# Performance work log

Measured on AMD Instinct MI355X. Metric: run time of the kernel, lower is better.

Reference implementation:

```python
import jax, jax.numpy as jnp
import numpy as np

L, H, NH, I = 6, 768, 12, 3072
DH = H // NH
EPS = 1e-12


def setup_inputs() -> dict:
    key = jax.random.key(0)
    ks = jax.random.split(key, 17)
    B, S = 16, 512
    s = lambda k, shape, fan: jax.random.normal(k, shape, jnp.float32) * (1.0 / np.sqrt(fan))
    return {
        "hidden_states": jax.random.normal(ks[0], (B, S, H), jnp.float32),
        "Wq": s(ks[1], (L, H, H), H), "bq": jnp.zeros((L, H), jnp.float32),
        "Wk": s(ks[2], (L, H, H), H), "bk": jnp.zeros((L, H), jnp.float32),
        "Wv": s(ks[3], (L, H, H), H), "bv": jnp.zeros((L, H), jnp.float32),
        "Wo": s(ks[4], (L, H, H), H), "bo": jnp.zeros((L, H), jnp.float32),
        "g1": jnp.ones((L, H), jnp.float32), "b1": jnp.zeros((L, H), jnp.float32),
        "Wi": s(ks[5], (L, H, I), H), "bi": jnp.zeros((L, I), jnp.float32),
        "Wo2": s(ks[6], (L, I, H), I), "bo2": jnp.zeros((L, H), jnp.float32),
        "g2": jnp.ones((L, H), jnp.float32), "b2": jnp.zeros((L, H), jnp.float32),
    }


def _layernorm(x, g, b):
    m = jnp.mean(x, axis=-1, keepdims=True)
    v = jnp.mean(jnp.square(x - m), axis=-1, keepdims=True)
    return (x - m) * jax.lax.rsqrt(v + EPS) * g + b


def _encoder(h, params):
    def layer_fn(h, p):
        Wq, bq, Wk, bk, Wv, bv, Wo, bo, g1, b1, Wi, bi, Wo2, bo2, g2, b2 = p
        B, S, _ = h.shape
        q = (h @ Wq + bq).reshape(B, S, NH, DH)
        k = (h @ Wk + bk).reshape(B, S, NH, DH)
        v = (h @ Wv + bv).reshape(B, S, NH, DH)
        scores = jnp.einsum("bshd,bthd->bhst", q, k) / np.sqrt(DH).astype(np.float32)
        probs = jax.nn.softmax(scores, axis=-1)  # dropout is identity in eval
        ctx = jnp.einsum("bhst,bthd->bshd", probs, v).reshape(B, S, H)
        attn_out = _layernorm(ctx @ Wo + bo + h, g1, b1)
        inter = jax.nn.gelu(attn_out @ Wi + bi, approximate=False)
        out = _layernorm(inter @ Wo2 + bo2 + attn_out, g2, b2)
        return out, None

    h, _ = jax.lax.scan(layer_fn, h, params)
    return h


def reference(hidden_states, Wq, bq, Wk, bk, Wv, bv, Wo, bo, g1, b1, Wi, bi, Wo2, bo2, g2, b2):
    params = (Wq, bq, Wk, bk, Wv, bv, Wo, bo, g1, b1, Wi, bi, Wo2, bo2, g2, b2)
    return _encoder(hidden_states, params)
```

## Files before the change

kernel.cpp:

```cpp
#include <hip/hip_runtime.h>
#include <hip/hip_bf16.h>
#include <math.h>

#define LNUM  6
#define HDIM  768
#define NHEAD 12
#define DHEAD 64
#define IDIM  3072
#define NB    16
#define SEQ   512
#define MTOK  (NB*SEQ)
#define NQKV  (3*HDIM)

typedef __bf16 bf16;
typedef __bf16 bf16x4 __attribute__((ext_vector_type(4)));
typedef __bf16 bf16x8 __attribute__((ext_vector_type(8)));
typedef float  f32x4  __attribute__((ext_vector_type(4)));

__device__ __forceinline__ void async_copy16(const bf16* g, bf16* l) {
  __builtin_amdgcn_global_load_lds((__attribute__((address_space(1))) void*)g,
                                   (__attribute__((address_space(3))) void*)l,
                                   16, 0, 0);
}

__device__ __forceinline__ float gelu_fast(float t) {
  const float u = 0.7978845608f * (t + 0.044715f * t * t * t);
  const float e = __expf(-2.f * fabsf(u));
  const float th = (1.f - e) / (1.f + e);
  return 0.5f * t * (1.f + copysignf(th, u));
}

__global__ void detect_k(const unsigned short* __restrict__ probe, int* __restrict__ flag)
{
  __shared__ int sc[4];
  const int tid = threadIdx.x;
  int cnt = 0;
#pragma unroll
  for (int j = 0; j < 16; j++) {
    const unsigned short w = probe[tid * 16 + j];
    const int e = (w >> 7) & 0xFF;
    cnt += (e >= 90 && e <= 130) ? 1 : 0;
  }
#pragma unroll
  for (int o = 32; o; o >>= 1) cnt += __shfl_xor(cnt, o);
  if ((tid & 63) == 0) sc[tid >> 6] = cnt;
  __syncthreads();
  if (tid == 0) flag[0] = ((sc[0] + sc[1] + sc[2] + sc[3]) < 3482) ? 1 : 0;
}

__global__ void cvt1d_k(const void* __restrict__ src, bf16* __restrict__ dst,
                        int n, const int* __restrict__ flag)
{
  const int i = blockIdx.x * 256 + threadIdx.x;
  if (i < n)
    dst[i] = (*flag) ? (bf16)((const float*)src)[i] : ((const bf16*)src)[i];
}

__global__ void cvt_slice_k(const void* __restrict__ src, bf16* __restrict__ dst,
                            int perL, int off, int dstStride, int total,
                            const int* __restrict__ flag)
{
  const int i = blockIdx.x * 256 + threadIdx.x;
  if (i < total) {
    const int l = i / perL, c = i - l * perL;
    const bf16 v = (*flag) ? (bf16)((const float*)src)[i] : ((const bf16*)src)[i];
    dst[l * dstStride + off + c] = v;
  }
}

__global__ void wtrans_k(const void* __restrict__ src, bf16* __restrict__ dst,
                         int K, int N, int layer, int dstLS, int dstOff,
                         const int* __restrict__ flag)
{
  __shared__ bf16 t[32][33];
  const size_t sOff = (size_t)(blockIdx.z + layer) * K * N;
  const size_t dOff = (size_t)blockIdx.z * dstLS + dstOff;
  const int n0 = blockIdx.x * 32, k0 = blockIdx.y * 32;
  const int tx = threadIdx.x, ty = threadIdx.y;
  const int f = *flag;
#pragma unroll
  for (int i = 0; i < 4; i++) {
    const size_t idx = sOff + (size_t)(k0 + ty*4 + i) * N + n0 + tx;
    t[ty*4+i][tx] = f ? (bf16)((const float*)src)[idx] : ((const bf16*)src)[idx];
  }
  __syncthreads();
#pragma unroll
  for (int i = 0; i < 4; i++)
    dst[dOff + (size_t)(n0 + ty*4 + i) * K + k0 + tx] = t[tx][ty*4+i];
}

template<int BM, int BN, int MT, int NT, int EPI, int XS>
__global__ __launch_bounds__(256)
void gemm_bt(const bf16* __restrict__ A, const bf16* __restrict__ Bt,
             float* __restrict__ Cf, bf16* __restrict__ Cb,
             bf16* __restrict__ Cb2, bf16* __restrict__ Cb3,
             const bf16* __restrict__ bias, const bf16* __restrict__ res,
             int K, int sA, int sB, int sC)
{
  __shared__ __align__(16) bf16 ldsA[BM*32];
  __shared__ __align__(16) bf16 ldsB[BN*32];
  const int tid  = threadIdx.x;
  const int wave = tid >> 6;
  const int lane = tid & 63;
  const int quad = lane >> 4;
  const int l16  = lane & 15;
  const int wm = wave >> 1, wn = wave & 1;
  const int swz = (l16 >> 1) & 3;

  int bx = blockIdx.x, by = blockIdx.y;
  if (XS) {
    if ((gridDim.y & 7) == 0) {
      const int id  = by * gridDim.x + bx;
      const int xcd = id & 7, slot = id >> 3;
      bx = slot % gridDim.x;
      by = (slot / gridDim.x) * 8 + xcd;
    }
  }
  const int m0 = by * BM;
  const int n0 = bx * BN;
  const int srow = tid >> 2;
  const int scol = (((tid & 3) ^ ((tid >> 3) & 3))) * 8;

  const bf16* gA = A + (size_t)(m0 + srow) * sA + scol;
  const bf16* gB = Bt + (size_t)(n0 + srow) * sB + scol;
  bf16* lA = &ldsA[(wave * 16) * 32];
  bf16* lB = &ldsB[(wave * 16) * 32];

  f32x4 acc[MT][NT];
  const f32x4 fzero = {0.f, 0.f, 0.f, 0.f};
#pragma unroll
  for (int i = 0; i < MT; i++)
#pragma unroll
    for (int j = 0; j < NT; j++) acc[i][j] = fzero;

  for (int k0 = 0; k0 < K; k0 += 32) {
#pragma unroll
    for (int p = 0; p < BM/64; p++)
      async_copy16(gA + (size_t)p * 64 * sA + k0, lA + p * 64 * 32);
#pragma unroll
    for (int p = 0; p < BN/64; p++)
      async_copy16(gB + (size_t)p * 64 * sB + k0, lB + p * 64 * 32);
    __syncthreads();

    bf16x8 af[MT], bfv[NT];
#pragma unroll
    for (int i = 0; i < MT; i++)
      af[i] = *(const bf16x8*)&ldsA[(wm*(MT*16) + i*16 + l16) * 32 + (quad ^ swz) * 8];
#pragma unroll
    for (int j = 0; j < NT; j++)
      bfv[j] = *(const bf16x8*)&ldsB[(wn*(NT*16) + j*16 + l16) * 32 + (quad ^ swz) * 8];
#pragma unroll
    for (int i = 0; i < MT; i++)
#pragma unroll
      for (int j = 0; j < NT; j++)
        acc[i][j] = __builtin_amdgcn_mfma_f32_16x16x32_bf16(af[i], bfv[j], acc[i][j], 0, 0, 0);
    __syncthreads();
  }

#pragma unroll
  for (int i = 0; i < MT; i++) {
    const int mtile = m0 + wm*(MT*16) + i*16 + quad*4;
#pragma unroll
    for (int j = 0; j < NT; j++) {
      const int nn = n0 + wn*(NT*16) + j*16 + l16;
      const float bv = bias ? (float)bias[nn] : 0.f;
      if (EPI == 5) {
        if (nn < HDIM) {
#pragma unroll
          for (int r = 0; r < 4; r++)
            Cb[(size_t)(mtile + r) * HDIM + nn] = (bf16)((acc[i][j][r] + bv) * 0.125f);
        } else if (nn < 2*HDIM) {
#pragma unroll
          for (int r = 0; r < 4; r++)
            Cb2[(size_t)(mtile + r) * HDIM + (nn - HDIM)] = (bf16)(acc[i][j][r] + bv);
        } else {
          const int nn2 = nn - 2*HDIM;
          const int bb = mtile >> 9, s = mtile & 511;
          const int hh = nn2 >> 6, dd = nn2 & 63;
          const size_t base = ((size_t)(bb*NHEAD + hh) * DHEAD + dd) * SEQ + s;
          bf16x4 pk;
#pragma unroll
          for (int r = 0; r < 4; r++) pk[r] = (bf16)(acc[i][j][r] + bv);
          *(bf16x4*)(Cb3 + base) = pk;
        }
      } else {
#pragma unroll
        for (int r = 0; r < 4; r++) {
          const int mm = mtile + r;
          const size_t idx = (size_t)mm * sC + nn;
          const float v = acc[i][j][r];
          if (EPI == 2) Cf[idx] = v + bv + (float)res[idx];
          else if (EPI == 3) Cb[idx] = (bf16)gelu_fast(v + bv);
        }
      }
    }
  }
}

#define STG_A(DST, h, kt2) do {                                               \
    async_copy16(gA + (size_t)((h)*128     ) * sA + (size_t)(kt2)*64,         \
                 &DST[(h)*8192 +        tid*8]);                              \
    async_copy16(gA + (size_t)((h)*128 + 64) * sA + (size_t)(kt2)*64,         \
                 &DST[(h)*8192 + 4096 + tid*8]);                              \
  } while (0)

#define STG_B(DST, h, kt2) do {                                               \
    async_copy16(gB + (size_t)((h)*128     ) * sB + (size_t)(kt2)*64,         \
                 &DST[(h)*8192 +        tid*8]);                              \
    async_copy16(gB + (size_t)((h)*128 + 64) * sB + (size_t)(kt2)*64,         \
                 &DST[(h)*8192 + 4096 + tid*8]);                              \
  } while (0)

#define MFMA16(ACI0, BREG, NOFF)                                              \
  __builtin_amdgcn_s_setprio(1);                                              \
  _Pragma("unroll")                                                           \
  for (int ks = 0; ks < 2; ks++)                                              \
    _Pragma("unroll")                                                         \
    for (int f = 0; f < 4; f++)                                               \
      _Pragma("unroll")                                                       \
      for (int nf = 0; nf < 2; nf++)                                          \
        acc[(ACI0) + f][(NOFF) + nf] =                                        \
            __builtin_amdgcn_mfma_f32_16x16x32_bf16(                          \
                aF[ks][f], BREG[ks][nf], acc[(ACI0) + f][(NOFF) + nf], 0,0,0);\
  __builtin_amdgcn_s_setprio(0);

#define DO_KTILE(AC, BC, STG0, STG1, STG2, STG3, ENDW)                        \
  {                                                                           \
                \
    _Pragma("unroll")                                                         \
    for (int f = 0; f < 4; f++) {                                             \
      const int row = (wm*128 + f*16 + l16) * 64;                             \
      aF[0][f] = *(const bf16x8*)&AC[row + sl0*8];                            \
      aF[1][f] = *(const bf16x8*)&AC[row + sl1*8];                            \
    }                                                                         \
    _Pragma("unroll")                                                         \
    for (int nf = 0; nf < 2; nf++) {                                          \
      const int row = (wn*64 + nf*16 + l16) * 64;                             \
      bA[0][nf] = *(const bf16x8*)&BC[row + sl0*8];                           \
      bA[1][nf] = *(const bf16x8*)&BC[row + sl1*8];                           \
    }                                                                         \
    STG0;                                                                     \
    asm volatile("s_waitcnt lgkmcnt(8)" ::: "memory");                        \
    __builtin_amdgcn_s_barrier();                                             \
    asm volatile("s_waitcnt lgkmcnt(0)" ::: "memory");                        \
    MFMA16(0, bA, 0)                                                          \
    __builtin_amdgcn_s_barrier();                                             \
                                    \
    _Pragma("unroll")                                                         \
    for (int nf = 0; nf < 2; nf++) {                                          \
      const int row = (wn*64 + 32 + nf*16 + l16) * 64;                        \
      bB[0][nf] = *(const bf16x8*)&BC[row + sl0*8];                           \
      bB[1][nf] = *(const bf16x8*)&BC[row + sl1*8];                           \
    }                                                                         \
    STG1;                                                                     \
    __builtin_amdgcn_s_barrier();                                             \
    asm volatile("s_waitcnt lgkmcnt(0)" ::: "memory");                        \
    MFMA16(0, bB, 2)                                                          \
    __builtin_amdgcn_s_barrier();                                             \
                          \
    _Pragma("unroll")                                                         \
    for (int f = 0; f < 4; f++) {                                             \
      const int row = (wm*128 + 64 + f*16 + l16) * 64;                        \
      aF[0][f] = *(const bf16x8*)&AC[row + sl0*8];                            \
      aF[1][f] = *(const bf16x8*)&AC[row + sl1*8];                            \
    }                                                                         \
    STG2;                                                                     \
    __builtin_amdgcn_s_barrier();                                             \
    asm volatile("s_waitcnt lgkmcnt(0)" ::: "memory");                        \
    MFMA16(4, bB, 2)                                                          \
    __builtin_amdgcn_s_barrier();                                             \
                                            \
    STG3;                                                                     \
    __builtin_amdgcn_s_barrier();                                             \
    MFMA16(4, bA, 0)                                                          \
    ENDW;                                                                     \
    __builtin_amdgcn_s_barrier();                                             \
  }

template<int EPI>
__global__ __launch_bounds__(512, 2)
void gemm256(const bf16* __restrict__ A, const bf16* __restrict__ Bt,
             float* __restrict__ Cf, bf16* __restrict__ Cb,
             bf16* __restrict__ Cb2, bf16* __restrict__ Cb3,
             const bf16* __restrict__ bias, const bf16* __restrict__ res,
             int K, int sA, int sB, int sC)
{
  __shared__ __align__(16) bf16 As0[256*64];
  __shared__ __align__(16) bf16 As1[256*64];
  __shared__ __align__(16) bf16 Bs0[256*64];
  __shared__ __align__(16) bf16 Bs1[256*64];

  const int tid  = threadIdx.x;
  const int wave = tid >> 6;
  const int lane = tid & 63;
  const int quad = lane >> 4;
  const int l16  = lane & 15;
  const int wm   = wave >> 2;
  const int wn   = wave & 3;

  int bx = blockIdx.x, by = blockIdx.y;
  if ((gridDim.y & 7) == 0) {
    const int id  = by * gridDim.x + bx;
    const int xcd = id & 7, slot = id >> 3;
    bx = slot % gridDim.x;
    by = (slot / gridDim.x) * 8 + xcd;
  }
  const int m0 = by * 256;
  const int n0 = bx * 256;

  const int rb  = tid >> 3;
  const int sb  = tid & 7;
  const int sbx = sb ^ (rb & 7);
  const bf16* gA = A  + (size_t)(m0 + rb) * sA + sbx * 8;
  const bf16* gB = Bt + (size_t)(n0 + rb) * sB + sbx * 8;

  const int s7  = l16 & 7;
  const int sl0 = (0 + quad) ^ s7;
  const int sl1 = (4 + quad) ^ s7;

  f32x4 acc[8][4];
  const f32x4 fzero = {0.f, 0.f, 0.f, 0.f};
#pragma unroll
  for (int i = 0; i < 8; i++)
#pragma unroll
    for (int j = 0; j < 4; j++) acc[i][j] = fzero;

  bf16x8 aF[2][4], bA[2][2], bB[2][2];

  const int NKT = K >> 6;

  STG_A(As0, 0, 0); STG_A(As0, 1, 0);
  STG_B(Bs0, 0, 0); STG_B(Bs0, 1, 0);
  if (NKT > 1) { STG_B(Bs1, 0, 1); STG_B(Bs1, 1, 1); }
  if (NKT > 1) asm volatile("s_waitcnt vmcnt(4)" ::: "memory");
  else         asm volatile("s_waitcnt vmcnt(0)" ::: "memory");
  __builtin_amdgcn_s_barrier();

  for (int kt = 0; kt < NKT; kt += 2) {
    const bool s2 = (kt + 2 < NKT);
    const bool s3 = (kt + 3 < NKT);
    DO_KTILE(As0, Bs0,
             STG_A(As1, 0, kt + 1),
             STG_A(As1, 1, kt + 1),
             if (s2) STG_B(Bs0, 0, kt + 2),
             if (s2) STG_B(Bs0, 1, kt + 2),
             if (s2) { asm volatile("s_waitcnt vmcnt(4)" ::: "memory"); }
             else    { asm volatile("s_waitcnt vmcnt(0)" ::: "memory"); })
    DO_KTILE(As1, Bs1,
             if (s2) STG_A(As0, 0, kt + 2),
             if (s2) STG_A(As0, 1, kt + 2),
             if (s3) STG_B(Bs1, 0, kt + 3),
             if (s3) STG_B(Bs1, 1, kt + 3),
             if (s2) { asm volatile("s_waitcnt vmcnt(4)" ::: "memory"); })
  }

#pragma unroll
  for (int mf = 0; mf < 8; mf++) {
    const int mtile = m0 + wm*128 + mf*16 + quad*4;
#pragma unroll
    for (int nf = 0; nf < 4; nf++) {
      const int nn = n0 + wn*64 + nf*16 + l16;
      const float bv = bias ? (float)bias[nn] : 0.f;
      if (EPI == 5) {
        if (nn < HDIM) {
#pragma unroll
          for (int r = 0; r < 4; r++)
            Cb[(size_t)(mtile + r) * HDIM + nn] = (bf16)((acc[mf][nf][r] + bv) * 0.125f);
        } else if (nn < 2*HDIM) {
#pragma unroll
          for (int r = 0; r < 4; r++)
            Cb2[(size_t)(mtile + r) * HDIM + (nn - HDIM)] = (bf16)(acc[mf][nf][r] + bv);
        } else {
          const int nn2 = nn - 2*HDIM;
          const int bb = mtile >> 9, s = mtile & 511;
          const int hh = nn2 >> 6, dd = nn2 & 63;
          const size_t base = ((size_t)(bb*NHEAD + hh) * DHEAD + dd) * SEQ + s;
          bf16x4 pk;
#pragma unroll
          for (int r = 0; r < 4; r++) pk[r] = (bf16)(acc[mf][nf][r] + bv);
          *(bf16x4*)(Cb3 + base) = pk;
        }
      } else if (EPI == 3) {
#pragma unroll
        for (int r = 0; r < 4; r++)
          Cb[(size_t)(mtile + r) * sC + nn] = (bf16)gelu_fast(acc[mf][nf][r] + bv);
      } else if (EPI == 2) {
#pragma unroll
        for (int r = 0; r < 4; r++) {
          const size_t idx = (size_t)(mtile + r) * sC + nn;
          Cf[idx] = acc[mf][nf][r] + bv + (float)res[idx];
        }
      }
    }
  }
}

__global__ __launch_bounds__(256)
void flash_k(const bf16* __restrict__ qb, const bf16* __restrict__ kb,
             const bf16* __restrict__ vt, bf16* __restrict__ ctxb)
{
  __shared__ __align__(16) bf16 Qs[128][72];
  __shared__ __align__(16) bf16 Ks[64][72];
  __shared__ __align__(16) bf16 Vs[64][72];
  __shared__ __align__(16) bf16 Ps[128][72];
  const int tid = threadIdx.x;
  const int wave = tid >> 6, lane = tid & 63;
  const int quad = lane >> 4, l16 = lane & 15;
  const int z = blockIdx.y;
  const int b = z / NHEAD, h = z - b * NHEAD;
  const int qt = blockIdx.x;
  const size_t qRow0 = (size_t)b * SEQ + qt * 128;

#pragma unroll
  for (int r = 0; r < 4; r++) {
    const int idx = tid + r * 256;
    const int row = idx >> 3, c8 = (idx & 7) * 8;
    *(bf16x8*)&Qs[row][c8] =
        *(const bf16x8*)&qb[(qRow0 + row) * HDIM + h * DHEAD + c8];
  }

  f32x4 Oacc[2][4];
  float mrow[2][4], lrow[2][4];
#pragma unroll
  for (int i = 0; i < 2; i++)
#pragma unroll
    for (int n = 0; n < 4; n++) Oacc[i][n] = (f32x4){0.f,0.f,0.f,0.f};
#pragma unroll
  for (int i = 0; i < 2; i++)
#pragma unroll
    for (int r = 0; r < 4; r++) { mrow[i][r] = -3.0e38f; lrow[i][r] = 0.f; }

  for (int j = 0; j < 8; j++) {
    __syncthreads();
#pragma unroll
    for (int r = 0; r < 2; r++) {
      const int idx = tid + r * 256;
      const int row = idx >> 3, c8 = (idx & 7) * 8;
      *(bf16x8*)&Ks[row][c8] =
          *(const bf16x8*)&kb[((size_t)b*SEQ + j*64 + row) * HDIM + h*DHEAD + c8];
      *(bf16x8*)&Vs[row][c8] =
          *(const bf16x8*)&vt[((size_t)z*DHEAD + row) * SEQ + j*64 + c8];
    }
    __syncthreads();

    f32x4 Sacc[2][4];
#pragma unroll
    for (int i = 0; i < 2; i++)
#pragma unroll
      for (int n = 0; n < 4; n++) Sacc[i][n] = (f32x4){0.f,0.f,0.f,0.f};
#pragma unroll
    for (int kk = 0; kk < 2; kk++) {
      bf16x8 af[2], bv[4];
#pragma unroll
      for (int i = 0; i < 2; i++)
        af[i] = *(const bf16x8*)&Qs[wave*32 + i*16 + l16][kk*32 + quad*8];
#pragma unroll
      for (int n = 0; n < 4; n++)
        bv[n] = *(const bf16x8*)&Ks[n*16 + l16][kk*32 + quad*8];
#pragma unroll
      for (int i = 0; i < 2; i++)
#pragma unroll
        for (int n = 0; n < 4; n++)
          Sacc[i][n] = __builtin_amdgcn_mfma_f32_16x16x32_bf16(af[i], bv[n], Sacc[i][n], 0,0,0);
    }

    float alpha[2][4];
#pragma unroll
    for (int i = 0; i < 2; i++)
#pragma unroll
      for (int r = 0; r < 4; r++) {
        float mx = Sacc[i][0][r];
#pragma unroll
        for (int n = 1; n < 4; n++) mx = fmaxf(mx, Sacc[i][n][r]);
#pragma unroll
        for (int o = 8; o; o >>= 1) mx = fmaxf(mx, __shfl_xor(mx, o));
        const float mn = fmaxf(mrow[i][r], mx);
        const float a = __expf(mrow[i][r] - mn);
        float rs = 0.f;
#pragma unroll
        for (int n = 0; n < 4; n++) {
          const float p = __expf(Sacc[i][n][r] - mn);
          Sacc[i][n][r] = p; rs += p;
        }
#pragma unroll
        for (int o = 8; o; o >>= 1) rs += __shfl_xor(rs, o);
        lrow[i][r] = lrow[i][r] * a + rs;
        mrow[i][r] = mn;
        alpha[i][r] = a;
      }

#pragma unroll
    for (int i = 0; i < 2; i++)
#pragma unroll
      for (int n = 0; n < 4; n++)
#pragma unroll
        for (int r = 0; r < 4; r++)
          Ps[wave*32 + i*16 + quad*4 + r][n*16 + l16] = (bf16)Sacc[i][n][r];
    __syncthreads();

#pragma unroll
    for (int i = 0; i < 2; i++)
#pragma unroll
      for (int n = 0; n < 4; n++)
#pragma unroll
        for (int r = 0; r < 4; r++) Oacc[i][n][r] *= alpha[i][r];
#pragma unroll
    for (int kk = 0; kk < 2; kk++) {
      bf16x8 af[2], bv[4];
#pragma unroll
      for (int i = 0; i < 2; i++)
        af[i] = *(const bf16x8*)&Ps[wave*32 + i*16 + l16][kk*32 + quad*8];
#pragma unroll
      for (int n = 0; n < 4; n++)
        bv[n] = *(const bf16x8*)&Vs[n*16 + l16][kk*32 + quad*8];
#pragma unroll
      for (int i = 0; i < 2; i++)
#pragma unroll
        for (int n = 0; n < 4; n++)
          Oacc[i][n] = __builtin_amdgcn_mfma_f32_16x16x32_bf16(af[i], bv[n], Oacc[i][n], 0,0,0);
    }
  }

#pragma unroll
  for (int i = 0; i < 2; i++)
#pragma unroll
    for (int r = 0; r < 4; r++) {
      const float inv = 1.f / lrow[i][r];
      const size_t tok = qRow0 + wave*32 + i*16 + quad*4 + r;
#pragma unroll
      for (int n = 0; n < 4; n++)
        ctxb[tok * HDIM + h*DHEAD + n*16 + l16] = (bf16)(Oacc[i][n][r] * inv);
    }
}

__global__ void layernorm_k(const float* __restrict__ x, const bf16* __restrict__ g,
                            const bf16* __restrict__ b, bf16* __restrict__ yb,
                            void* __restrict__ dout, int last, const int* __restrict__ flag)
{
  __shared__ float sred[4];
  const int row = blockIdx.x;
  const int tid = threadIdx.x;
  const float* xr = x + (size_t)row * HDIM;
  const float v0 = xr[tid], v1 = xr[tid+256], v2 = xr[tid+512];
  float s = v0 + v1 + v2;
#pragma unroll
  for (int o = 32; o; o >>= 1) s += __shfl_xor(s, o);
  if ((tid & 63) == 0) sred[tid >> 6] = s;
  __syncthreads();
  const float mean = (sred[0]+sred[1]+sred[2]+sred[3]) * (1.f/768.f);
  __syncthreads();
  const float d0 = v0-mean, d1 = v1-mean, d2 = v2-mean;
  float vs = d0*d0 + d1*d1 + d2*d2;
#pragma unroll
  for (int o = 32; o; o >>= 1) vs += __shfl_xor(vs, o);
  if ((tid & 63) == 0) sred[tid >> 6] = vs;
  __syncthreads();
  const float var = (sred[0]+sred[1]+sred[2]+sred[3]) * (1.f/768.f);
  const float rs  = rsqrtf(var + 1e-12f);
  const float y0 = d0*rs*(float)g[tid]     + (float)b[tid];
  const float y1 = d1*rs*(float)g[tid+256] + (float)b[tid+256];
  const float y2 = d2*rs*(float)g[tid+512] + (float)b[tid+512];
  bf16* ybr = yb + (size_t)row * HDIM;
  ybr[tid]     = (bf16)y0;
  ybr[tid+256] = (bf16)y1;
  ybr[tid+512] = (bf16)y2;
  if (last) {
    if (*flag) {
      float* o = (float*)dout + (size_t)row * HDIM;
      o[tid] = y0; o[tid+256] = y1; o[tid+512] = y2;
    } else {
      bf16* o = (bf16*)dout + (size_t)row * HDIM;
      o[tid] = (bf16)y0; o[tid+256] = (bf16)y1; o[tid+512] = (bf16)y2;
    }
  }
}

extern "C" void kernel_launch(void* const* d_in, const int* in_sizes, int n_in,
                              void* d_out, int out_size, void* d_ws, size_t ws_size,
                              hipStream_t stream)
{
  (void)in_sizes; (void)n_in; (void)out_size;

  char* ws = (char*)d_ws;
  size_t off = 0;
  auto carve = [&](size_t bytes) -> char* {
    char* p = ws + off; off += (bytes + 255) & ~(size_t)255; return p;
  };
  int*   flag = (int*)carve(256);
  bf16*  hcur = (bf16*)carve((size_t)MTOK*HDIM*2);
  bf16*  qb   = (bf16*)carve((size_t)MTOK*HDIM*2);
  bf16*  kb   = (bf16*)carve((size_t)MTOK*HDIM*2);
  bf16*  vt   = (bf16*)carve((size_t)MTOK*HDIM*2);
  bf16*  ctxb = (bf16*)carve((size_t)MTOK*HDIM*2);
  float* x1   = (float*)carve((size_t)MTOK*HDIM*4);
  bf16*  aob  = kb;

  bf16* nbqkv = (bf16*)carve((size_t)LNUM*NQKV*2);
  bf16* nbo   = (bf16*)carve((size_t)LNUM*HDIM*2);
  bf16* ng1   = (bf16*)carve((size_t)LNUM*HDIM*2);
  bf16* nb1   = (bf16*)carve((size_t)LNUM*HDIM*2);
  bf16* nbi   = (bf16*)carve((size_t)LNUM*IDIM*2);
  bf16* nbo2  = (bf16*)carve((size_t)LNUM*HDIM*2);
  bf16* ng2   = (bf16*)carve((size_t)LNUM*HDIM*2);
  bf16* nb2   = (bf16*)carve((size_t)LNUM*HDIM*2);

  const size_t wAllBytes = (size_t)LNUM*(NQKV*HDIM + HDIM*HDIM + 2*HDIM*IDIM)*2;
  const bool preAll = ws_size >= off + wAllBytes + (size_t)256*IDIM*2 + (1u<<20);
  bf16 *wqkvt=0, *wot=0, *wit=0, *wo2t=0, *bufA=0, *bufB=0;
  if (preAll) {
    wqkvt = (bf16*)carve((size_t)LNUM*NQKV*HDIM*2);
    wot   = (bf16*)carve((size_t)LNUM*HDIM*HDIM*2);
    wit   = (bf16*)carve((size_t)LNUM*HDIM*IDIM*2);
    wo2t  = (bf16*)carve((size_t)LNUM*HDIM*IDIM*2);
  } else {
    bufA = (bf16*)carve((size_t)HDIM*IDIM*2);
    bufB = (bf16*)carve((size_t)HDIM*IDIM*2);
  }

  const size_t unionAvail = (ws_size > off) ? (ws_size - off) : 0;
  int RM = 256;
  { const int rms[6] = {8192,4096,2048,1024,512,256};
    for (int i = 0; i < 6; i++)
      if ((size_t)rms[i]*IDIM*2 <= unionAvail) { RM = rms[i]; break; } }
  bf16* interb = (bf16*)(ws + off);

  detect_k<<<1, 256, 0, stream>>>((const unsigned short*)d_in[1], flag);
  cvt1d_k<<<(MTOK*HDIM+255)/256, 256, 0, stream>>>(d_in[0], hcur, MTOK*HDIM, flag);
  cvt_slice_k<<<(LNUM*HDIM+255)/256, 256, 0, stream>>>(d_in[2], nbqkv, HDIM, 0,      NQKV, LNUM*HDIM, flag);
  cvt_slice_k<<<(LNUM*HDIM+255)/256, 256, 0, stream>>>(d_in[4], nbqkv, HDIM, HDIM,   NQKV, LNUM*HDIM, flag);
  cvt_slice_k<<<(LNUM*HDIM+255)/256, 256, 0, stream>>>(d_in[6], nbqkv, HDIM, 2*HDIM, NQKV, LNUM*HDIM, flag);
  cvt1d_k<<<(LNUM*HDIM+255)/256, 256, 0, stream>>>(d_in[8],  nbo,  LNUM*HDIM, flag);
  cvt1d_k<<<(LNUM*HDIM+255)/256, 256, 0, stream>>>(d_in[9],  ng1,  LNUM*HDIM, flag);
  cvt1d_k<<<(LNUM*HDIM+255)/256, 256, 0, stream>>>(d_in[10], nb1,  LNUM*HDIM, flag);
  cvt1d_k<<<(LNUM*IDIM+255)/256, 256, 0, stream>>>(d_in[12], nbi,  LNUM*IDIM, flag);
  cvt1d_k<<<(LNUM*HDIM+255)/256, 256, 0, stream>>>(d_in[14], nbo2, LNUM*HDIM, flag);
  cvt1d_k<<<(LNUM*HDIM+255)/256, 256, 0, stream>>>(d_in[15], ng2,  LNUM*HDIM, flag);
  cvt1d_k<<<(LNUM*HDIM+255)/256, 256, 0, stream>>>(d_in[16], nb2,  LNUM*HDIM, flag);

  const dim3 tb(32, 8);
  if (preAll) {
    wtrans_k<<<dim3(HDIM/32, HDIM/32, LNUM), tb, 0, stream>>>(d_in[1], wqkvt, HDIM, HDIM, 0, NQKV*HDIM, 0,           flag);
    wtrans_k<<<dim3(HDIM/32, HDIM/32, LNUM), tb, 0, stream>>>(d_in[3], wqkvt, HDIM, HDIM, 0, NQKV*HDIM, HDIM*HDIM,   flag);
    wtrans_k<<<dim3(HDIM/32, HDIM/32, LNUM), tb, 0, stream>>>(d_in[5], wqkvt, HDIM, HDIM, 0, NQKV*HDIM, 2*HDIM*HDIM, flag);
    wtrans_k<<<dim3(HDIM/32, HDIM/32, LNUM), tb, 0, stream>>>(d_in[7], wot,  HDIM, HDIM, 0, HDIM*HDIM, 0, flag);
    wtrans_k<<<dim3(IDIM/32, HDIM/32, LNUM), tb, 0, stream>>>(d_in[11], wit,  HDIM, IDIM, 0, HDIM*IDIM, 0, flag);
    wtrans_k<<<dim3(HDIM/32, IDIM/32, LNUM), tb, 0, stream>>>(d_in[13], wo2t, IDIM, HDIM, 0, HDIM*IDIM, 0, flag);
  }

  for (int l = 0; l < LNUM; l++) {
    const bf16* hin = hcur;

    const bf16* WqkvT;
    if (preAll) WqkvT = wqkvt + (size_t)l * NQKV * HDIM;
    else {
      wtrans_k<<<dim3(HDIM/32, HDIM/32, 1), tb, 0, stream>>>(d_in[1], bufA, HDIM, HDIM, l, 0, 0,           flag);
      wtrans_k<<<dim3(HDIM/32, HDIM/32, 1), tb, 0, stream>>>(d_in[3], bufA, HDIM, HDIM, l, 0, HDIM*HDIM,   flag);
      wtrans_k<<<dim3(HDIM/32, HDIM/32, 1), tb, 0, stream>>>(d_in[5], bufA, HDIM, HDIM, l, 0, 2*HDIM*HDIM, flag);
      WqkvT = bufA;
    }
    gemm256<5><<<dim3(NQKV/256, MTOK/256), 512, 0, stream>>>(
        hin, WqkvT, nullptr, qb, kb, vt, nbqkv + (size_t)l*NQKV, nullptr,
        HDIM, HDIM, HDIM, HDIM);

    flash_k<<<dim3(SEQ/128, NB*NHEAD), 256, 0, stream>>>(qb, kb, vt, ctxb);

    const bf16* WoT;
    if (preAll) WoT = wot + (size_t)l * HDIM * HDIM;
    else {
      wtrans_k<<<dim3(HDIM/32, HDIM/32, 1), tb, 0, stream>>>(d_in[7], bufA, HDIM, HDIM, l, 0, 0, flag);
      WoT = bufA;
    }
    gemm_bt<128,128,4,4,2,1><<<dim3(HDIM/128, MTOK/128), 256, 0, stream>>>(
        ctxb, WoT, x1, nullptr, nullptr, nullptr, nbo + l*HDIM, hin,
        HDIM, HDIM, HDIM, HDIM);
    layernorm_k<<<MTOK, 256, 0, stream>>>(x1, ng1 + l*HDIM, nb1 + l*HDIM, aob,
                                          d_out, 0, flag);

    const bf16 *WiT, *Wo2T;
    if (preAll) { WiT = wit + (size_t)l*HDIM*IDIM; Wo2T = wo2t + (size_t)l*HDIM*IDIM; }
    else {
      wtrans_k<<<dim3(IDIM/32, HDIM/32, 1), tb, 0, stream>>>(d_in[11], bufA, HDIM, IDIM, l, 0, 0, flag);
      wtrans_k<<<dim3(HDIM/32, IDIM/32, 1), tb, 0, stream>>>(d_in[13], bufB, IDIM, HDIM, l, 0, 0, flag);
      WiT = bufA; Wo2T = bufB;
    }
    for (int r0 = 0; r0 < MTOK; r0 += RM) {
      gemm256<3><<<dim3(IDIM/256, RM/256), 512, 0, stream>>>(
          aob + (size_t)r0*HDIM, WiT, nullptr, interb, nullptr, nullptr,
          nbi + (size_t)l*IDIM, nullptr, HDIM, HDIM, HDIM, IDIM);
      gemm_bt<128,128,4,4,2,1><<<dim3(HDIM/128, RM/128), 256, 0, stream>>>(
          interb, Wo2T, x1 + (size_t)r0*HDIM, nullptr, nullptr, nullptr,
          nbo2 + l*HDIM, aob + (size_t)r0*HDIM, IDIM, IDIM, IDIM, HDIM);
    }
    layernorm_k<<<MTOK, 256, 0, stream>>>(x1, ng2 + l*HDIM, nb2 + l*HDIM, hcur,
                                          d_out, (l == LNUM-1) ? 1 : 0, flag);
  }
}
```

Baseline: 2.215 ms.

## Double-buffer gemm_bt LDS and replace gemm256 with it for QKV and FFN-up

Adds a two-stage LDS ping-pong to gemm_bt, so async global-to-LDS copies for the next K slice are issued before the MFMAs on the current slice, hiding load latency. It then deletes the hand-scheduled 256x256 gemm256 kernel and routes the QKV and FFN-up GEMMs through the 128x128 gemm_bt instead. This trades the larger tile's data reuse and fine-grained barrier schedule for a simpler kernel with more blocks. The loop assumes K is a multiple of 64.

```diff
diff --git a/kernel.cpp b/kernel.cpp
--- a/kernel.cpp
+++ b/kernel.cpp
@@ -89,6 +89,35 @@
     dst[dOff + (size_t)(n0 + ty*4 + i) * K + k0 + tx] = t[tx][ty*4+i];
 }
 
+#define STAGE2(DA, DB, KK) do {                                                \
+    _Pragma("unroll")                                                          \
+    for (int p = 0; p < BM/64; p++)                                            \
+      async_copy16(gA + (size_t)p * 64 * sA + (KK),                            \
+                   &DA[(wave*16)*32 + p*64*32]);                               \
+    _Pragma("unroll")                                                          \
+    for (int p = 0; p < BN/64; p++)                                            \
+      async_copy16(gB + (size_t)p * 64 * sB + (KK),                            \
+                   &DB[(wave*16)*32 + p*64*32]);                               \
+  } while (0)
+
+#define COMP2(SA, SB) do {                                                     \
+    bf16x8 af[MT], bfv[NT];                                                    \
+    _Pragma("unroll")                                                          \
+    for (int i = 0; i < MT; i++)                                               \
+      af[i] = *(const bf16x8*)&SA[(wm*(MT*16) + i*16 + l16) * 32               \
+                                  + (quad ^ swz) * 8];                         \
+    _Pragma("unroll")                                                          \
+    for (int j = 0; j < NT; j++)                                               \
+      bfv[j] = *(const bf16x8*)&SB[(wn*(NT*16) + j*16 + l16) * 32              \
+                                   + (quad ^ swz) * 8];                        \
+    _Pragma("unroll")                                                          \
+    for (int i = 0; i < MT; i++)                                               \
+      _Pragma("unroll")                                                        \
+      for (int j = 0; j < NT; j++)                                             \
+        acc[i][j] = __builtin_amdgcn_mfma_f32_16x16x32_bf16(                   \
+            af[i], bfv[j], acc[i][j], 0, 0, 0);                                \
+  } while (0)
+
 template<int BM, int BN, int MT, int NT, int EPI, int XS>
 __global__ __launch_bounds__(256)
 void gemm_bt(const bf16* __restrict__ A, const bf16* __restrict__ Bt,
@@ -97,8 +126,10 @@
              const bf16* __restrict__ bias, const bf16* __restrict__ res,
              int K, int sA, int sB, int sC)
 {
-  __shared__ __align__(16) bf16 ldsA[BM*32];
-  __shared__ __align__(16) bf16 ldsB[BN*32];
+  __shared__ __align__(16) bf16 A0[BM*32];
+  __shared__ __align__(16) bf16 B0[BN*32];
+  __shared__ __align__(16) bf16 A1[BM*32];
+  __shared__ __align__(16) bf16 B1[BN*32];
   const int tid  = threadIdx.x;
   const int wave = tid >> 6;
   const int lane = tid & 63;
@@ -123,8 +154,6 @@
 
   const bf16* gA = A + (size_t)(m0 + srow) * sA + scol;
   const bf16* gB = Bt + (size_t)(n0 + srow) * sB + scol;
-  bf16* lA = &ldsA[(wave * 16) * 32];
-  bf16* lB = &ldsB[(wave * 16) * 32];
 
   f32x4 acc[MT][NT];
   const f32x4 fzero = {0.f, 0.f, 0.f, 0.f};
@@ -133,27 +162,14 @@
 #pragma unroll
     for (int j = 0; j < NT; j++) acc[i][j] = fzero;
 
-  for (int k0 = 0; k0 < K; k0 += 32) {
-#pragma unroll
-    for (int p = 0; p < BM/64; p++)
-      async_copy16(gA + (size_t)p * 64 * sA + k0, lA + p * 64 * 32);
-#pragma unroll
-    for (int p = 0; p < BN/64; p++)
-      async_copy16(gB + (size_t)p * 64 * sB + k0, lB + p * 64 * 32);
+  STAGE2(A0, B0, 0);
+  __syncthreads();
+  for (int k0 = 0; k0 < K; k0 += 64) {
+    STAGE2(A1, B1, k0 + 32);
+    COMP2(A0, B0);
     __syncthreads();
-
-    bf16x8 af[MT], bfv[NT];
-#pragma unroll
-    for (int i = 0; i < MT; i++)
-      af[i] = *(const bf16x8*)&ldsA[(wm*(MT*16) + i*16 + l16) * 32 + (quad ^ swz) * 8];
-#pragma unroll
-    for (int j = 0; j < NT; j++)
-      bfv[j] = *(const bf16x8*)&ldsB[(wn*(NT*16) + j*16 + l16) * 32 + (quad ^ swz) * 8];
-#pragma unroll
-    for (int i = 0; i < MT; i++)
-#pragma unroll
-      for (int j = 0; j < NT; j++)
-        acc[i][j] = __builtin_amdgcn_mfma_f32_16x16x32_bf16(af[i], bfv[j], acc[i][j], 0, 0, 0);
+    if (k0 + 64 < K) STAGE2(A0, B0, k0 + 64);
+    COMP2(A1, B1);
     __syncthreads();
   }
 
@@ -191,204 +207,6 @@
           const float v = acc[i][j][r];
           if (EPI == 2) Cf[idx] = v + bv + (float)res[idx];
           else if (EPI == 3) Cb[idx] = (bf16)gelu_fast(v + bv);
-        }
-      }
-    }
-  }
-}
-
-#define STG_A(DST, h, kt2) do {                                               \
-    async_copy16(gA + (size_t)((h)*128     ) * sA + (size_t)(kt2)*64,         \
-                 &DST[(h)*8192 +        tid*8]);                              \
-    async_copy16(gA + (size_t)((h)*128 + 64) * sA + (size_t)(kt2)*64,         \
-                 &DST[(h)*8192 + 4096 + tid*8]);                              \
-  } while (0)
-
-#define STG_B(DST, h, kt2) do {                                               \
-    async_copy16(gB + (size_t)((h)*128     ) * sB + (size_t)(kt2)*64,         \
-                 &DST[(h)*8192 +        tid*8]);                              \
-    async_copy16(gB + (size_t)((h)*128 + 64) * sB + (size_t)(kt2)*64,         \
-                 &DST[(h)*8192 + 4096 + tid*8]);                              \
-  } while (0)
-
-#define MFMA16(ACI0, BREG, NOFF)                                              \
-  __builtin_amdgcn_s_setprio(1);                                              \
-  _Pragma("unroll")                                                           \
-  for (int ks = 0; ks < 2; ks++)                                              \
-    _Pragma("unroll")                                                         \
-    for (int f = 0; f < 4; f++)                                               \
-      _Pragma("unroll")                                                       \
-      for (int nf = 0; nf < 2; nf++)                                          \
-        acc[(ACI0) + f][(NOFF) + nf] =                                        \
-            __builtin_amdgcn_mfma_f32_16x16x32_bf16(                          \
-                aF[ks][f], BREG[ks][nf], acc[(ACI0) + f][(NOFF) + nf], 0,0,0);\
-  __builtin_amdgcn_s_setprio(0);
-
-#define DO_KTILE(AC, BC, STG0, STG1, STG2, STG3, ENDW)                        \
-  {                                                                           \
-                \
-    _Pragma("unroll")                                                         \
-    for (int f = 0; f < 4; f++) {                                             \
-      const int row = (wm*128 + f*16 + l16) * 64;                             \
-      aF[0][f] = *(const bf16x8*)&AC[row + sl0*8];                            \
-      aF[1][f] = *(const bf16x8*)&AC[row + sl1*8];                            \
-    }                                                                         \
-    _Pragma("unroll")                                                         \
-    for (int nf = 0; nf < 2; nf++) {                                          \
-      const int row = (wn*64 + nf*16 + l16) * 64;                             \
-      bA[0][nf] = *(const bf16x8*)&BC[row + sl0*8];                           \
-      bA[1][nf] = *(const bf16x8*)&BC[row + sl1*8];                           \
-    }                                                                         \
-    STG0;                                                                     \
-    asm volatile("s_waitcnt lgkmcnt(8)" ::: "memory");                        \
-    __builtin_amdgcn_s_barrier();                                             \
-    asm volatile("s_waitcnt lgkmcnt(0)" ::: "memory");                        \
-    MFMA16(0, bA, 0)                                                          \
-    __builtin_amdgcn_s_barrier();                                             \
-                                    \
-    _Pragma("unroll")                                                         \
-    for (int nf = 0; nf < 2; nf++) {                                          \
-      const int row = (wn*64 + 32 + nf*16 + l16) * 64;                        \
-      bB[0][nf] = *(const bf16x8*)&BC[row + sl0*8];                           \
-      bB[1][nf] = *(const bf16x8*)&BC[row + sl1*8];                           \
-    }                                                                         \
-    STG1;                                                                     \
-    __builtin_amdgcn_s_barrier();                                             \
-    asm volatile("s_waitcnt lgkmcnt(0)" ::: "memory");                        \
-    MFMA16(0, bB, 2)                                                          \
-    __builtin_amdgcn_s_barrier();                                             \
-                          \
-    _Pragma("unroll")                                                         \
-    for (int f = 0; f < 4; f++) {                                             \
-      const int row = (wm*128 + 64 + f*16 + l16) * 64;                        \
-      aF[0][f] = *(const bf16x8*)&AC[row + sl0*8];                            \
-      aF[1][f] = *(const bf16x8*)&AC[row + sl1*8];                            \
-    }                                                                         \
-    STG2;                                                                     \
-    __builtin_amdgcn_s_barrier();                                             \
-    asm volatile("s_waitcnt lgkmcnt(0)" ::: "memory");                        \
-    MFMA16(4, bB, 2)                                                          \
-    __builtin_amdgcn_s_barrier();                                             \
-                                            \
-    STG3;                                                                     \
-    __builtin_amdgcn_s_barrier();                                             \
-    MFMA16(4, bA, 0)                                                          \
-    ENDW;                                                                     \
-    __builtin_amdgcn_s_barrier();                                             \
-  }
-
-template<int EPI>
-__global__ __launch_bounds__(512, 2)
-void gemm256(const bf16* __restrict__ A, const bf16* __restrict__ Bt,
-             float* __restrict__ Cf, bf16* __restrict__ Cb,
-             bf16* __restrict__ Cb2, bf16* __restrict__ Cb3,
-             const bf16* __restrict__ bias, const bf16* __restrict__ res,
-             int K, int sA, int sB, int sC)
-{
-  __shared__ __align__(16) bf16 As0[256*64];
-  __shared__ __align__(16) bf16 As1[256*64];
-  __shared__ __align__(16) bf16 Bs0[256*64];
-  __shared__ __align__(16) bf16 Bs1[256*64];
-
-  const int tid  = threadIdx.x;
-  const int wave = tid >> 6;
-  const int lane = tid & 63;
-  const int quad = lane >> 4;
-  const int l16  = lane & 15;
-  const int wm   = wave >> 2;
-  const int wn   = wave & 3;
-
-  int bx = blockIdx.x, by = blockIdx.y;
-  if ((gridDim.y & 7) == 0) {
-    const int id  = by * gridDim.x + bx;
-    const int xcd = id & 7, slot = id >> 3;
-    bx = slot % gridDim.x;
-    by = (slot / gridDim.x) * 8 + xcd;
-  }
-  const int m0 = by * 256;
-  const int n0 = bx * 256;
-
-  const int rb  = tid >> 3;
-  const int sb  = tid & 7;
-  const int sbx = sb ^ (rb & 7);
-  const bf16* gA = A  + (size_t)(m0 + rb) * sA + sbx * 8;
-  const bf16* gB = Bt + (size_t)(n0 + rb) * sB + sbx * 8;
-
-  const int s7  = l16 & 7;
-  const int sl0 = (0 + quad) ^ s7;
-  const int sl1 = (4 + quad) ^ s7;
-
-  f32x4 acc[8][4];
-  const f32x4 fzero = {0.f, 0.f, 0.f, 0.f};
-#pragma unroll
-  for (int i = 0; i < 8; i++)
-#pragma unroll
-    for (int j = 0; j < 4; j++) acc[i][j] = fzero;
-
-  bf16x8 aF[2][4], bA[2][2], bB[2][2];
-
-  const int NKT = K >> 6;
-
-  STG_A(As0, 0, 0); STG_A(As0, 1, 0);
-  STG_B(Bs0, 0, 0); STG_B(Bs0, 1, 0);
-  if (NKT > 1) { STG_B(Bs1, 0, 1); STG_B(Bs1, 1, 1); }
-  if (NKT > 1) asm volatile("s_waitcnt vmcnt(4)" ::: "memory");
-  else         asm volatile("s_waitcnt vmcnt(0)" ::: "memory");
-  __builtin_amdgcn_s_barrier();
-
-  for (int kt = 0; kt < NKT; kt += 2) {
-    const bool s2 = (kt + 2 < NKT);
-    const bool s3 = (kt + 3 < NKT);
-    DO_KTILE(As0, Bs0,
-             STG_A(As1, 0, kt + 1),
-             STG_A(As1, 1, kt + 1),
-             if (s2) STG_B(Bs0, 0, kt + 2),
-             if (s2) STG_B(Bs0, 1, kt + 2),
-             if (s2) { asm volatile("s_waitcnt vmcnt(4)" ::: "memory"); }
-             else    { asm volatile("s_waitcnt vmcnt(0)" ::: "memory"); })
-    DO_KTILE(As1, Bs1,
-             if (s2) STG_A(As0, 0, kt + 2),
-             if (s2) STG_A(As0, 1, kt + 2),
-             if (s3) STG_B(Bs1, 0, kt + 3),
-             if (s3) STG_B(Bs1, 1, kt + 3),
-             if (s2) { asm volatile("s_waitcnt vmcnt(4)" ::: "memory"); })
-  }
-
-#pragma unroll
-  for (int mf = 0; mf < 8; mf++) {
-    const int mtile = m0 + wm*128 + mf*16 + quad*4;
-#pragma unroll
-    for (int nf = 0; nf < 4; nf++) {
-      const int nn = n0 + wn*64 + nf*16 + l16;
-      const float bv = bias ? (float)bias[nn] : 0.f;
-      if (EPI == 5) {
-        if (nn < HDIM) {
-#pragma unroll
-          for (int r = 0; r < 4; r++)
-            Cb[(size_t)(mtile + r) * HDIM + nn] = (bf16)((acc[mf][nf][r] + bv) * 0.125f);
-        } else if (nn < 2*HDIM) {
-#pragma unroll
-          for (int r = 0; r < 4; r++)
-            Cb2[(size_t)(mtile + r) * HDIM + (nn - HDIM)] = (bf16)(acc[mf][nf][r] + bv);
-        } else {
-          const int nn2 = nn - 2*HDIM;
-          const int bb = mtile >> 9, s = mtile & 511;
-          const int hh = nn2 >> 6, dd = nn2 & 63;
-          const size_t base = ((size_t)(bb*NHEAD + hh) * DHEAD + dd) * SEQ + s;
-          bf16x4 pk;
-#pragma unroll
-          for (int r = 0; r < 4; r++) pk[r] = (bf16)(acc[mf][nf][r] + bv);
-          *(bf16x4*)(Cb3 + base) = pk;
-        }
-      } else if (EPI == 3) {
-#pragma unroll
-        for (int r = 0; r < 4; r++)
-          Cb[(size_t)(mtile + r) * sC + nn] = (bf16)gelu_fast(acc[mf][nf][r] + bv);
-      } else if (EPI == 2) {
-#pragma unroll
-        for (int r = 0; r < 4; r++) {
-          const size_t idx = (size_t)(mtile + r) * sC + nn;
-          Cf[idx] = acc[mf][nf][r] + bv + (float)res[idx];
         }
       }
     }
@@ -658,7 +476,7 @@
       wtrans_k<<<dim3(HDIM/32, HDIM/32, 1), tb, 0, stream>>>(d_in[5], bufA, HDIM, HDIM, l, 0, 2*HDIM*HDIM, flag);
       WqkvT = bufA;
     }
-    gemm256<5><<<dim3(NQKV/256, MTOK/256), 512, 0, stream>>>(
+    gemm_bt<128,128,4,4,5,1><<<dim3(NQKV/128, MTOK/128), 256, 0, stream>>>(
         hin, WqkvT, nullptr, qb, kb, vt, nbqkv + (size_t)l*NQKV, nullptr,
         HDIM, HDIM, HDIM, HDIM);
 
@@ -684,7 +502,7 @@
       WiT = bufA; Wo2T = bufB;
     }
     for (int r0 = 0; r0 < MTOK; r0 += RM) {
-      gemm256<3><<<dim3(IDIM/256, RM/256), 512, 0, stream>>>(
+      gemm_bt<128,128,4,4,3,1><<<dim3(IDIM/128, RM/128), 256, 0, stream>>>(
           aob + (size_t)r0*HDIM, WiT, nullptr, interb, nullptr, nullptr,
           nbi + (size_t)l*IDIM, nullptr, HDIM, HDIM, HDIM, IDIM);
       gemm_bt<128,128,4,4,2,1><<<dim3(HDIM/128, RM/128), 256, 0, stream>>>(
```

Measured after the change: 2.056 ms. 7.2% less time.
